# Kernel tuning notes

Measured on AMD Instinct MI355X. Metric: run time of the kernel, lower is better.

The kernel has to match this reference:

```python
import jax, jax.numpy as jnp
import numpy as np

SIGMA = 0.25  # self.sigmas in RBFDynamics


def setup_inputs() -> dict:
    key = jax.random.key(0)
    k1, k2, k3 = jax.random.split(key, 3)
    N, C, D, M = 100000, 256, 2, 5
    x = jax.random.normal(k1, (N, D), dtype=jnp.float32)
    centers = jax.random.normal(k2, (C, D), dtype=jnp.float32)
    weights = jax.random.normal(k3, (M, C, D), dtype=jnp.float32)
    return {"x": x, "centers": centers, "weights": weights}


def reference(x, centers, weights):
    x2 = jnp.sum(x * x, axis=-1, keepdims=True)          # [N, 1]
    c2 = jnp.sum(centers * centers, axis=-1)             # [C]
    d2 = x2 + c2[None, :] - 2.0 * (x @ centers.T)        # [N, C]
    d2 = jnp.maximum(d2, 0.0)
    # torch: exp(-cdist(x, centers)**2) * sigmas**2
    rbf = jnp.exp(-d2) * (SIGMA * SIGMA)                 # [N, C]
    # per-model matmul with weights, batched across ensemble -> [M, N, D]
    out = jnp.einsum('nc,mcd->mnd', rbf, weights)
    return out
```

## Files before the change

kernel.cpp:

```cpp
#include <hip/hip_runtime.h>

#if __has_builtin(__builtin_amdgcn_exp2f)
__device__ __forceinline__ float fast_exp2(float x) { return __builtin_amdgcn_exp2f(x); }
#else
__device__ __forceinline__ float fast_exp2(float x) { return exp2f(x); }
#endif

constexpr int C_ = 256;
constexpr int M_ = 5;
constexpr float LOG2E = 1.4426950408889634f;

__global__ __launch_bounds__(256, 8) void ensemble_rbf_kernel(
    const float* __restrict__ x,
    const float* __restrict__ centers,
    const float* __restrict__ weights,
    float* __restrict__ out,
    int N)
{
    __shared__ float s_tab[C_ * 12];

    const int tid   = threadIdx.x;
    const int nl    = tid & 63;
    const int chunk = tid >> 6;

    {
        float2 cv = ((const float2*)centers)[tid];
        float c2  = fmaf(cv.x, cv.x, cv.y * cv.y);
        float s   = fast_exp2(fmaf(c2, -LOG2E, -4.0f));
        float* row = &s_tab[tid * 12];
        row[0] = (2.0f * LOG2E) * cv.x;
        row[1] = (2.0f * LOG2E) * cv.y;
        const float2* w2 = (const float2*)weights;
        #pragma unroll
        for (int m = 0; m < M_; m++) {
            float2 wv = w2[m * C_ + tid];
            row[2 + 2 * m]     = wv.x * s;
            row[2 + 2 * m + 1] = wv.y * s;
        }
    }
    __syncthreads();

    const int n = blockIdx.x * 64 + nl;
    float2 xv = (n < N) ? ((const float2*)x)[n] : make_float2(0.f, 0.f);

    float acc[2 * M_];
    #pragma unroll
    for (int i = 0; i < 2 * M_; i++) acc[i] = 0.f;

    const float4* tab4 = (const float4*)s_tab;
    const int cbase = chunk * 64;

    #pragma unroll 4
    for (int cc = 0; cc < 64; cc++) {
        int c = cbase + cc;
        float4 t0 = tab4[c * 3 + 0];
        float4 t1 = tab4[c * 3 + 1];
        float4 t2 = tab4[c * 3 + 2];

        float r = fast_exp2(fmaf(xv.y, t0.y, xv.x * t0.x));

        acc[0] = fmaf(r, t0.z, acc[0]);  acc[1] = fmaf(r, t0.w, acc[1]);
        acc[2] = fmaf(r, t1.x, acc[2]);  acc[3] = fmaf(r, t1.y, acc[3]);
        acc[4] = fmaf(r, t1.z, acc[4]);  acc[5] = fmaf(r, t1.w, acc[5]);
        acc[6] = fmaf(r, t2.x, acc[6]);  acc[7] = fmaf(r, t2.y, acc[7]);
        acc[8] = fmaf(r, t2.z, acc[8]);  acc[9] = fmaf(r, t2.w, acc[9]);
    }

    __syncthreads();
    {
        float4* slot = (float4*)&s_tab[(chunk * 64 + nl) * 12];
        slot[0] = make_float4(acc[0], acc[1], acc[2], acc[3]);
        slot[1] = make_float4(acc[4], acc[5], acc[6], acc[7]);
        slot[2] = make_float4(acc[8], acc[9], 0.f, 0.f);
    }
    __syncthreads();

    if (tid < 64 && n < N) {
        float4 s0 = make_float4(0.f, 0.f, 0.f, 0.f);
        float4 s1 = s0, s2 = s0;
        #pragma unroll
        for (int k = 0; k < 4; k++) {
            const float4* slot = (const float4*)&s_tab[(k * 64 + nl) * 12];
            float4 r0 = slot[0], r1 = slot[1], r2 = slot[2];
            s0.x += r0.x; s0.y += r0.y; s0.z += r0.z; s0.w += r0.w;
            s1.x += r1.x; s1.y += r1.y; s1.z += r1.z; s1.w += r1.w;
            s2.x += r2.x; s2.y += r2.y;
        }
        float x2    = fmaf(xv.x, xv.x, xv.y * xv.y);
        float scale = fast_exp2(x2 * -LOG2E);

        float2* out2 = (float2*)out;
        out2[(size_t)0 * N + n] = make_float2(s0.x * scale, s0.y * scale);
        out2[(size_t)1 * N + n] = make_float2(s0.z * scale, s0.w * scale);
        out2[(size_t)2 * N + n] = make_float2(s1.x * scale, s1.y * scale);
        out2[(size_t)3 * N + n] = make_float2(s1.z * scale, s1.w * scale);
        out2[(size_t)4 * N + n] = make_float2(s2.x * scale, s2.y * scale);
    }
}

extern "C" void kernel_launch(void* const* d_in, const int* in_sizes, int n_in,
                              void* d_out, int out_size, void* d_ws, size_t ws_size,
                              hipStream_t stream) {
    const float* x       = (const float*)d_in[0];
    const float* centers = (const float*)d_in[1];
    const float* weights = (const float*)d_in[2];
    float* out = (float*)d_out;

    int N = in_sizes[0] / 2;
    int grid = (N + 63) / 64;
    ensemble_rbf_kernel<<<grid, 256, 0, stream>>>(x, centers, weights, out, N);
}
```

Baseline: 70.19 us.

## Register-block four points per thread to reuse LDS table reads

Each thread now processes four points instead of one, so every shared-memory table row read for a center is reused across four exp/FMA chains. Blocks cover 256 points, which cuts the number of blocks and the repeated per-block table setup to a quarter. The final reduction now uses all 256 threads, each reading x again to compute the scale. In exchange the kernel uses 40 accumulators per thread and 48KB of shared memory, with launch bounds lowered to 2, so occupancy drops.

```diff
diff --git a/kernel.cpp b/kernel.cpp
--- a/kernel.cpp
+++ b/kernel.cpp
@@ -10,84 +10,104 @@
 constexpr int M_ = 5;
 constexpr float LOG2E = 1.4426950408889634f;
 
-__global__ __launch_bounds__(256, 8) void ensemble_rbf_kernel(
+__global__ __launch_bounds__(256, 2) void ensemble_rbf_kernel(
     const float* __restrict__ x,
     const float* __restrict__ centers,
     const float* __restrict__ weights,
     float* __restrict__ out,
     int N)
 {
-    __shared__ float s_tab[C_ * 12];
+    __shared__ float s_mem[4 * C_ * 12];
 
-    const int tid   = threadIdx.x;
-    const int nl    = tid & 63;
-    const int chunk = tid >> 6;
+    const int tid  = threadIdx.x;
+    const int lane = tid & 63;
+    const int wv   = tid >> 6;
 
     {
         float2 cv = ((const float2*)centers)[tid];
         float c2  = fmaf(cv.x, cv.x, cv.y * cv.y);
         float s   = fast_exp2(fmaf(c2, -LOG2E, -4.0f));
-        float* row = &s_tab[tid * 12];
+        float* row = &s_mem[tid * 12];
         row[0] = (2.0f * LOG2E) * cv.x;
         row[1] = (2.0f * LOG2E) * cv.y;
         const float2* w2 = (const float2*)weights;
         #pragma unroll
         for (int m = 0; m < M_; m++) {
-            float2 wv = w2[m * C_ + tid];
-            row[2 + 2 * m]     = wv.x * s;
-            row[2 + 2 * m + 1] = wv.y * s;
+            float2 wvv = w2[m * C_ + tid];
+            row[2 + 2 * m]     = wvv.x * s;
+            row[2 + 2 * m + 1] = wvv.y * s;
         }
     }
     __syncthreads();
 
-    const int n = blockIdx.x * 64 + nl;
-    float2 xv = (n < N) ? ((const float2*)x)[n] : make_float2(0.f, 0.f);
+    const int nbase = blockIdx.x * 256;
+    const int n0    = nbase + 4 * lane;
 
-    float acc[2 * M_];
+    float2 xv[4];
+    if (n0 + 3 < N) {
+        const float4* x4 = (const float4*)x;
+        float4 a = x4[(nbase >> 1) + 2 * lane];
+        float4 b = x4[(nbase >> 1) + 2 * lane + 1];
+        xv[0] = make_float2(a.x, a.y);
+        xv[1] = make_float2(a.z, a.w);
+        xv[2] = make_float2(b.x, b.y);
+        xv[3] = make_float2(b.z, b.w);
+    } else {
+        #pragma unroll
+        for (int j = 0; j < 4; j++)
+            xv[j] = (n0 + j < N) ? ((const float2*)x)[n0 + j]
+                                 : make_float2(0.f, 0.f);
+    }
+
+    float acc[4][10];
     #pragma unroll
-    for (int i = 0; i < 2 * M_; i++) acc[i] = 0.f;
+    for (int j = 0; j < 4; j++)
+        #pragma unroll
+        for (int k = 0; k < 10; k++) acc[j][k] = 0.f;
 
-    const float4* tab4 = (const float4*)s_tab;
-    const int cbase = chunk * 64;
+    const float4* tab4 = (const float4*)s_mem;
+    const int cb3 = wv * 64 * 3;
 
     #pragma unroll 4
     for (int cc = 0; cc < 64; cc++) {
-        int c = cbase + cc;
-        float4 t0 = tab4[c * 3 + 0];
-        float4 t1 = tab4[c * 3 + 1];
-        float4 t2 = tab4[c * 3 + 2];
-
-        float r = fast_exp2(fmaf(xv.y, t0.y, xv.x * t0.x));
-
-        acc[0] = fmaf(r, t0.z, acc[0]);  acc[1] = fmaf(r, t0.w, acc[1]);
-        acc[2] = fmaf(r, t1.x, acc[2]);  acc[3] = fmaf(r, t1.y, acc[3]);
-        acc[4] = fmaf(r, t1.z, acc[4]);  acc[5] = fmaf(r, t1.w, acc[5]);
-        acc[6] = fmaf(r, t2.x, acc[6]);  acc[7] = fmaf(r, t2.y, acc[7]);
-        acc[8] = fmaf(r, t2.z, acc[8]);  acc[9] = fmaf(r, t2.w, acc[9]);
+        float4 t0 = tab4[cb3 + cc * 3 + 0];
+        float4 t1 = tab4[cb3 + cc * 3 + 1];
+        float4 t2 = tab4[cb3 + cc * 3 + 2];
+        const float w[10] = {t0.z, t0.w, t1.x, t1.y, t1.z,
+                             t1.w, t2.x, t2.y, t2.z, t2.w};
+        #pragma unroll
+        for (int j = 0; j < 4; j++) {
+            float r = fast_exp2(fmaf(xv[j].y, t0.y, xv[j].x * t0.x));
+            #pragma unroll
+            for (int k = 0; k < 10; k++)
+                acc[j][k] = fmaf(r, w[k], acc[j][k]);
+        }
     }
 
     __syncthreads();
-    {
-        float4* slot = (float4*)&s_tab[(chunk * 64 + nl) * 12];
-        slot[0] = make_float4(acc[0], acc[1], acc[2], acc[3]);
-        slot[1] = make_float4(acc[4], acc[5], acc[6], acc[7]);
-        slot[2] = make_float4(acc[8], acc[9], 0.f, 0.f);
+    #pragma unroll
+    for (int j = 0; j < 4; j++) {
+        float4* slot = (float4*)&s_mem[(wv * C_ + 4 * lane + j) * 12];
+        slot[0] = make_float4(acc[j][0], acc[j][1], acc[j][2], acc[j][3]);
+        slot[1] = make_float4(acc[j][4], acc[j][5], acc[j][6], acc[j][7]);
+        slot[2] = make_float4(acc[j][8], acc[j][9], 0.f, 0.f);
     }
     __syncthreads();
 
-    if (tid < 64 && n < N) {
+    const int n = nbase + tid;
+    if (n < N) {
         float4 s0 = make_float4(0.f, 0.f, 0.f, 0.f);
         float4 s1 = s0, s2 = s0;
         #pragma unroll
         for (int k = 0; k < 4; k++) {
-            const float4* slot = (const float4*)&s_tab[(k * 64 + nl) * 12];
+            const float4* slot = (const float4*)&s_mem[(k * C_ + tid) * 12];
             float4 r0 = slot[0], r1 = slot[1], r2 = slot[2];
             s0.x += r0.x; s0.y += r0.y; s0.z += r0.z; s0.w += r0.w;
             s1.x += r1.x; s1.y += r1.y; s1.z += r1.z; s1.w += r1.w;
             s2.x += r2.x; s2.y += r2.y;
         }
-        float x2    = fmaf(xv.x, xv.x, xv.y * xv.y);
-        float scale = fast_exp2(x2 * -LOG2E);
+        float2 xn   = ((const float2*)x)[n];
+        float scale = fast_exp2(fmaf(xn.x, xn.x, xn.y * xn.y) * -LOG2E);
 
         float2* out2 = (float2*)out;
         out2[(size_t)0 * N + n] = make_float2(s0.x * scale, s0.y * scale);
@@ -107,6 +127,6 @@
     float* out = (float*)d_out;
 
     int N = in_sizes[0] / 2;
-    int grid = (N + 63) / 64;
+    int grid = (N + 255) / 256;
     ensemble_rbf_kernel<<<grid, 256, 0, stream>>>(x, centers, weights, out, N);
 }
```

Result: no change. 70.96 us (+1.1%).
